# Kernel optimization log

Hardware: AMD Instinct MI355X
Metric: run time of the kernel (lower is better)

## Reference

```python
import jax, jax.numpy as jnp
import numpy as np

T, N, D, E = 4, 50000, 32, 800000
V_TH = 1.0      # v_threshold
ALPHA = 4.0     # surrogate-gradient sharpness


def setup_inputs() -> dict:
    key = jax.random.key(0)
    k1, k2, k3, k4 = jax.random.split(key, 4)
    s_seq = jax.random.normal(k1, (T, N, D), dtype=jnp.float32) * 0.5
    z_seq = jax.random.normal(k2, (N, D), dtype=jnp.float32) * 0.5
    edge_index = jax.random.randint(k3, (2, E), 0, N, dtype=jnp.int64)
    # GCNConv weight (bias=False), Glorot-ish scale
    W = jax.random.normal(k4, (D, D), dtype=jnp.float32) / np.sqrt(D).astype(np.float32)
    return {"s_seq": s_seq, "z_seq": z_seq, "W": W, "edge_index": edge_index}


def _gcn_conv(x, W, edge_index, n_nodes):
    """PyG GCNConv with add_self_loops=True, normalize=True, bias=False.
    x: [T,N,D]; returns [T,N,D]."""
    src, dst = edge_index[0], edge_index[1]
    ones = jnp.ones(src.shape[0], dtype=x.dtype)
    deg = jax.ops.segment_sum(ones, dst, num_segments=n_nodes) + 1.0  # +1 self loop
    dinv = jax.lax.rsqrt(deg)                                        # [N]
    xw = jnp.einsum('tnd,df->tnf', x, W)                             # dense transform
    norm = dinv[src] * dinv[dst]                                     # [E]
    msgs = xw[:, src, :] * norm[None, :, None]                       # [T,E,D] gather
    agg = jax.vmap(lambda m: jax.ops.segment_sum(m, dst, num_segments=n_nodes))(msgs)
    # self-loop contribution with norm dinv[i]^2
    return agg + xw * (dinv * dinv)[None, :, None]


def _spike(v):
    # Heaviside spike with surrogate (sigmoid) gradient, straight-through.
    s = (v >= V_TH).astype(v.dtype)
    sg = jax.nn.sigmoid(ALPHA * (v - V_TH))
    return s + sg - jax.lax.stop_gradient(sg)


def reference(s_seq, z_seq, W, edge_index):
    n_nodes = s_seq.shape[1]
    x_seq = _gcn_conv(s_seq, W, edge_index, n_nodes)   # [T,N,D]  (dropout p=0.0 is identity)
    y_seq = x_seq.mean(0)                              # temporal mean [N,D]
    # Riemannian IF node: integrate-and-fire over time with soft reset;
    # latent state z drifts by the temporal mean (Euclidean proxy for expmap).
    def step(v, x_t):
        v = v + x_t
        o = _spike(v)
        v = v - o * V_TH
        return v, o
    v0 = jnp.zeros_like(z_seq)
    _, o_seq = jax.lax.scan(step, v0, x_seq)           # [T,N,D]
    z_new = z_seq + y_seq
    return o_seq, z_new
```

## Files before the change

### kernel.cpp

```cpp
#include <hip/hip_runtime.h>
#include <hip/hip_fp16.h>

#define TSTEPS 4
#define DIM 32
#define BINW_SHIFT 8
#define NB 256
#define SP_CH 2048
#define NCHP 400
#define PAD_PER_BIN 772

typedef _Float16 f16x8 __attribute__((ext_vector_type(8)));
typedef float f32x4 __attribute__((ext_vector_type(4)));

__device__ __forceinline__ void ldx8h(const __half* p, float4& lo, float4& hi) {
    uint4 u = *(const uint4*)p;
    __half2 h0 = *(__half2*)&u.x;
    __half2 h1 = *(__half2*)&u.y;
    __half2 h2 = *(__half2*)&u.z;
    __half2 h3 = *(__half2*)&u.w;
    float2 a = __half22float2(h0);
    float2 b = __half22float2(h1);
    float2 c = __half22float2(h2);
    float2 d = __half22float2(h3);
    lo = make_float4(a.x, a.y, b.x, b.y);
    hi = make_float4(c.x, c.y, d.x, d.y);
}

__global__ __launch_bounds__(256) void hist_kernel(
    const int* __restrict__ ei, int* __restrict__ ghistT, int E) {
    __shared__ int lh[NB];
    int tid = threadIdx.x;
    lh[tid] = 0;
    __syncthreads();
    int beg = blockIdx.x * SP_CH;
    int end = min(beg + SP_CH, E);
    for (int e = beg + tid; e < end; e += 256)
        atomicAdd(&lh[ei[E + e] >> BINW_SHIFT], 1);
    __syncthreads();
    ghistT[tid * NCHP + blockIdx.x] = lh[tid];
}

__global__ __launch_bounds__(512) void colscan_kernel(
    const int* __restrict__ ghistT, int* __restrict__ ghist2,
    int* __restrict__ totals, int nchunks) {
    __shared__ int sc[512];
    int t = threadIdx.x;
    int b = blockIdx.x;
    int v = (t < nchunks) ? ghistT[b * NCHP + t] : 0;
    sc[t] = v;
    __syncthreads();
    for (int off = 1; off < 512; off <<= 1) {
        int tv = (t >= off) ? sc[t - off] : 0;
        __syncthreads();
        sc[t] += tv;
        __syncthreads();
    }
    if (t < nchunks) ghist2[(size_t)t * NB + b] = sc[t] - v;
    if (t == 511) totals[b] = sc[511];
}

__global__ __launch_bounds__(256) void splitgemm_kernel(
    const int* __restrict__ ei, const int* __restrict__ ghist2,
    const int* __restrict__ totals, unsigned int* __restrict__ esorted,
    int* __restrict__ binScanG,
    const float* __restrict__ s, const float* __restrict__ W,
    __half* __restrict__ xwp, int E, int rows, int N, int nchunks) {
    __shared__ __align__(16) char smem[4352];
    int tid = threadIdx.x;

    if ((int)blockIdx.x < nchunks) {
        int* sBS  = (int*)smem;
        int* gb   = (int*)(smem + 1024);
        int* lcur = (int*)(smem + 2048);
        int bid = blockIdx.x;
        int tot = totals[tid];
        sBS[tid] = tot;
        __syncthreads();
        for (int off = 1; off < 256; off <<= 1) {
            int t = (tid >= off) ? sBS[tid - off] : 0;
            __syncthreads();
            sBS[tid] += t;
            __syncthreads();
        }
        if (bid == 0) binScanG[tid] = sBS[tid];
        gb[tid] = (sBS[tid] - tot) + ghist2[(size_t)bid * NB + tid];
        lcur[tid] = 0;
        __syncthreads();
        int beg = bid * SP_CH;
        int end = min(beg + SP_CH, E);
        for (int e = beg + tid; e < end; e += 256) {
            int sx = ei[e];
            int dx = ei[E + e];
            unsigned int pk = (unsigned int)sx | ((unsigned int)dx << 16);
            int b = dx >> BINW_SHIFT;
            int p = atomicAdd(&lcur[b], 1);
            esorted[gb[b] + p] = pk;
        }
        return;
    }

    float (*Wf)[33] = (float(*)[33])smem;
    {
        float4 wv = ((const float4*)W)[tid];
        int kk = tid >> 3, c4 = (tid & 7) * 4;
        Wf[kk][c4 + 0] = wv.x; Wf[kk][c4 + 1] = wv.y;
        Wf[kk][c4 + 2] = wv.z; Wf[kk][c4 + 3] = wv.w;
    }
    __syncthreads();

    int lane = tid & 63;
    int wid  = tid >> 6;
    int lrow = lane & 15;
    int kq   = lane >> 4;
    int k0   = kq * 8;

    f16x8 b0, b1;
#pragma unroll
    for (int i = 0; i < 8; i++) {
        b0[i] = (_Float16)Wf[k0 + i][lrow];
        b1[i] = (_Float16)Wf[k0 + i][lrow + 16];
    }

    int rbase = ((int)blockIdx.x - nchunks) * 128 + wid * 32;
#pragma unroll
    for (int rt = 0; rt < 2; rt++) {
        int r = rbase + rt * 16 + lrow;
        f16x8 a;
        if (r < rows) {
            const float4* sp = (const float4*)(s + (size_t)r * 32 + k0);
            float4 u0 = sp[0], u1 = sp[1];
            a[0] = (_Float16)u0.x; a[1] = (_Float16)u0.y;
            a[2] = (_Float16)u0.z; a[3] = (_Float16)u0.w;
            a[4] = (_Float16)u1.x; a[5] = (_Float16)u1.y;
            a[6] = (_Float16)u1.z; a[7] = (_Float16)u1.w;
        } else {
#pragma unroll
            for (int i = 0; i < 8; i++) a[i] = (_Float16)0.f;
        }
        f32x4 c0 = {0.f, 0.f, 0.f, 0.f};
        f32x4 c1 = {0.f, 0.f, 0.f, 0.f};
        c0 = __builtin_amdgcn_mfma_f32_16x16x32_f16(b0, a, c0, 0, 0, 0);
        c1 = __builtin_amdgcn_mfma_f32_16x16x32_f16(b1, a, c1, 0, 0, 0);
        if (r < rows) {
            int t = (r >= 3 * N) ? 3 : (r >= 2 * N) ? 2 : (r >= N) ? 1 : 0;
            int n = r - t * N;
            __half2 p0 = __floats2half2_rn(c0[0], c0[1]);
            __half2 p1 = __floats2half2_rn(c0[2], c0[3]);
            __half2 p2 = __floats2half2_rn(c1[0], c1[1]);
            __half2 p3 = __floats2half2_rn(c1[2], c1[3]);
            __half* dst = xwp + (size_t)n * 128 + t * 32;
            uint2 u0, u1;
            u0.x = *(unsigned int*)&p0; u0.y = *(unsigned int*)&p1;
            u1.x = *(unsigned int*)&p2; u1.y = *(unsigned int*)&p3;
            *(uint2*)(dst + kq * 4)      = u0;
            *(uint2*)(dst + 16 + kq * 4) = u1;
        }
    }
}

__global__ __launch_bounds__(512) void csr_kernel(
    const int* __restrict__ binScanG, const unsigned int* __restrict__ esorted,
    int* __restrict__ rec, int* __restrict__ offs, int* __restrict__ deg,
    float* __restrict__ dinv, __half* __restrict__ xwp, int N) {
    __shared__ int lh[NB], sc[NB], loff[NB], lcur[NB];
    __shared__ float sdi[NB];
    int bin = blockIdx.x;
    int tid = threadIdx.x;
    int e0 = bin ? binScanG[bin - 1] : 0;
    int e1 = binScanG[bin];
    int ebeg = e0;
    int cnt = e1 - e0;
    if (tid < NB) lh[tid] = 0;
    __syncthreads();
    int gbase = ((ebeg + 3) & ~3) + PAD_PER_BIN * bin;
    for (int i = tid; i < cnt; i += 512)
        atomicAdd(&lh[(esorted[ebeg + i] >> 16) & 255], 1);
    __syncthreads();
    int padded = 0;
    if (tid < NB) {
        sdi[tid] = rsqrtf((float)lh[tid] + 1.0f);
        padded = (lh[tid] + 3) & ~3;
        sc[tid] = padded;
    }
    __syncthreads();
    for (int off = 1; off < 256; off <<= 1) {
        int t = (tid >= off && tid < NB) ? sc[tid - off] : 0;
        __syncthreads();
        if (tid < NB) sc[tid] += t;
        __syncthreads();
    }
    if (tid < NB) {
        loff[tid] = sc[tid] - padded;
        lcur[tid] = 0;
    }
    __syncthreads();
    for (int i = tid; i < cnt; i += 512) {
        unsigned int e = esorted[ebeg + i];
        int ln = (e >> 16) & 255;
        int p = atomicAdd(&lcur[ln], 1);
        rec[gbase + loff[ln] + p] = (int)(e & 0xFFFFu);
    }
    int n = (bin << BINW_SHIFT) + tid;
    if (tid < NB && n < N) {
        offs[n] = gbase + loff[tid];
        deg[n] = lh[tid];
        dinv[n] = sdi[tid];
    }
    {
        int hbase = bin << 15;
        int limit = min(32768, N * 128 - hbase);
        __half* slab = xwp + hbase;
        for (int i = tid; i * 8 < limit; i += 512) {
            float di = sdi[i >> 4];
            uint4 u = *(uint4*)(slab + i * 8);
            __half2 h0 = *(__half2*)&u.x;
            __half2 h1 = *(__half2*)&u.y;
            __half2 h2 = *(__half2*)&u.z;
            __half2 h3 = *(__half2*)&u.w;
            float2 f0 = __half22float2(h0);
            float2 f1 = __half22float2(h1);
            float2 f2 = __half22float2(h2);
            float2 f3 = __half22float2(h3);
            h0 = __floats2half2_rn(f0.x * di, f0.y * di);
            h1 = __floats2half2_rn(f1.x * di, f1.y * di);
            h2 = __floats2half2_rn(f2.x * di, f2.y * di);
            h3 = __floats2half2_rn(f3.x * di, f3.y * di);
            u.x = *(unsigned int*)&h0;
            u.y = *(unsigned int*)&h1;
            u.z = *(unsigned int*)&h2;
            u.w = *(unsigned int*)&h3;
            *(uint4*)(slab + i * 8) = u;
        }
    }
}

__global__ __launch_bounds__(256) void gather_kernel(
    const int* __restrict__ rec, const int* __restrict__ offs,
    const int* __restrict__ deg, const __half* __restrict__ xwp,
    const float* __restrict__ dinv, const float* __restrict__ z,
    float* __restrict__ out, int N) {
    int gid = blockIdx.x * 256 + threadIdx.x;
    int n = gid >> 4;
    if (n >= N) return;
    int wl = threadIdx.x & 63;
    int g = wl >> 4;
    int l = wl & 15;
    long lofs = (long)l * 8;

    float dn = dinv[n];
    int beg = offs[n];
    int cntn = deg[n];

    float4 aLo = make_float4(0.f, 0.f, 0.f, 0.f);
    float4 aHi = make_float4(0.f, 0.f, 0.f, 0.f);
    int i = 0;
    for (; i + 8 <= cntn; i += 8) {
        int4 sa = *(const int4*)(rec + beg + i);
        int4 sb = *(const int4*)(rec + beg + i + 4);
        float4 l0, h0, l1, h1, l2, h2, l3, h3;
        float4 l4, h4, l5, h5, l6, h6, l7, h7;
        ldx8h(xwp + (long)sa.x * 128 + lofs, l0, h0);
        ldx8h(xwp + (long)sa.y * 128 + lofs, l1, h1);
        ldx8h(xwp + (long)sa.z * 128 + lofs, l2, h2);
        ldx8h(xwp + (long)sa.w * 128 + lofs, l3, h3);
        ldx8h(xwp + (long)sb.x * 128 + lofs, l4, h4);
        ldx8h(xwp + (long)sb.y * 128 + lofs, l5, h5);
        ldx8h(xwp + (long)sb.z * 128 + lofs, l6, h6);
        ldx8h(xwp + (long)sb.w * 128 + lofs, l7, h7);
        aLo.x += (l0.x + l1.x) + (l2.x + l3.x) + (l4.x + l5.x) + (l6.x + l7.x);
        aLo.y += (l0.y + l1.y) + (l2.y + l3.y) + (l4.y + l5.y) + (l6.y + l7.y);
        aLo.z += (l0.z + l1.z) + (l2.z + l3.z) + (l4.z + l5.z) + (l6.z + l7.z);
        aLo.w += (l0.w + l1.w) + (l2.w + l3.w) + (l4.w + l5.w) + (l6.w + l7.w);
        aHi.x += (h0.x + h1.x) + (h2.x + h3.x) + (h4.x + h5.x) + (h6.x + h7.x);
        aHi.y += (h0.y + h1.y) + (h2.y + h3.y) + (h4.y + h5.y) + (h6.y + h7.y);
        aHi.z += (h0.z + h1.z) + (h2.z + h3.z) + (h4.z + h5.z) + (h6.z + h7.z);
        aHi.w += (h0.w + h1.w) + (h2.w + h3.w) + (h4.w + h5.w) + (h6.w + h7.w);
    }
    for (; i < cntn; i += 4) {
        int4 s4 = *(const int4*)(rec + beg + i);
        int rem = cntn - i;
        int i0 = s4.x;
        int i1 = (rem > 1) ? s4.y : i0;
        int i2 = (rem > 2) ? s4.z : i0;
        int i3 = (rem > 3) ? s4.w : i0;
        float w1 = (rem > 1) ? 1.f : 0.f;
        float w2 = (rem > 2) ? 1.f : 0.f;
        float w3 = (rem > 3) ? 1.f : 0.f;
        float4 l0, h0, l1, h1, l2, h2, l3, h3;
        ldx8h(xwp + (long)i0 * 128 + lofs, l0, h0);
        ldx8h(xwp + (long)i1 * 128 + lofs, l1, h1);
        ldx8h(xwp + (long)i2 * 128 + lofs, l2, h2);
        ldx8h(xwp + (long)i3 * 128 + lofs, l3, h3);
        aLo.x += l0.x + w1 * l1.x + w2 * l2.x + w3 * l3.x;
        aLo.y += l0.y + w1 * l1.y + w2 * l2.y + w3 * l3.y;
        aLo.z += l0.z + w1 * l1.z + w2 * l2.z + w3 * l3.z;
        aLo.w += l0.w + w1 * l1.w + w2 * l2.w + w3 * l3.w;
        aHi.x += h0.x + w1 * h1.x + w2 * h2.x + w3 * h3.x;
        aHi.y += h0.y + w1 * h1.y + w2 * h2.y + w3 * h3.y;
        aHi.z += h0.z + w1 * h1.z + w2 * h2.z + w3 * h3.z;
        aHi.w += h0.w + w1 * h1.w + w2 * h2.w + w3 * h3.w;
    }
    {
        float4 sl, sh;
        ldx8h(xwp + (long)n * 128 + lofs, sl, sh);
        aLo.x += sl.x; aLo.y += sl.y; aLo.z += sl.z; aLo.w += sl.w;
        aHi.x += sh.x; aHi.y += sh.y; aHi.z += sh.z; aHi.w += sh.w;
    }
    aLo.x *= dn; aLo.y *= dn; aLo.z *= dn; aLo.w *= dn;
    aHi.x *= dn; aHi.y *= dn; aHi.z *= dn; aHi.w *= dn;

    float a8[8] = {aLo.x, aLo.y, aLo.z, aLo.w, aHi.x, aHi.y, aHi.z, aHi.w};
    float xs[TSTEPS][8];
    int base = g * 16;
#pragma unroll
    for (int t = 0; t < TSTEPS; t++) {
        int srcLane = base + t * 4 + l;
#pragma unroll
        for (int j = 0; j < 8; j++)
            xs[t][j] = __shfl(a8[j], srcLane, 64);
    }
    if (l < 4) {
        int colBase = n * 32 + l * 8;
        float v[8], y[8];
#pragma unroll
        for (int j = 0; j < 8; j++) {
            v[j] = 0.f;
            y[j] = (xs[0][j] + xs[1][j] + xs[2][j] + xs[3][j]) * 0.25f;
        }
#pragma unroll
        for (int t = 0; t < TSTEPS; t++) {
            float o[8];
#pragma unroll
            for (int j = 0; j < 8; j++) {
                v[j] += xs[t][j];
                o[j] = (v[j] >= 1.0f) ? 1.0f : 0.0f;
                v[j] -= o[j];
            }
            float* dst = out + (size_t)t * N * 32 + colBase;
            *(float4*)dst       = make_float4(o[0], o[1], o[2], o[3]);
            *(float4*)(dst + 4) = make_float4(o[4], o[5], o[6], o[7]);
        }
        float4 zv0 = *(const float4*)(z + colBase);
        float4 zv1 = *(const float4*)(z + colBase + 4);
        float* dst = out + (size_t)TSTEPS * N * 32 + colBase;
        *(float4*)dst       = make_float4(zv0.x + y[0], zv0.y + y[1], zv0.z + y[2], zv0.w + y[3]);
        *(float4*)(dst + 4) = make_float4(zv1.x + y[4], zv1.y + y[5], zv1.z + y[6], zv1.w + y[7]);
    }
}

extern "C" void kernel_launch(void* const* d_in, const int* in_sizes, int n_in,
                              void* d_out, int out_size, void* d_ws, size_t ws_size,
                              hipStream_t stream) {
    const float* s_seq = (const float*)d_in[0];
    const float* z_seq = (const float*)d_in[1];
    const float* W     = (const float*)d_in[2];
    const int*   ei    = (const int*)d_in[3];
    float* out = (float*)d_out;

    int N = in_sizes[1] / DIM;
    int E = in_sizes[3] / 2;
    int rows = TSTEPS * N;
    int nb = (N + 255) >> BINW_SHIFT;
    int nchunks = (E + SP_CH - 1) / SP_CH;

    char* w = (char*)d_ws;
    __half* xwp           = (__half*)w;       w += (size_t)rows * DIM * 2;
    unsigned int* esorted = (unsigned int*)w; w += (size_t)E * 4;
    int*   rec     = (int*)w;  w += ((size_t)E + PAD_PER_BIN * nb + 16) * 4;
    int*   offs    = (int*)w;  w += (size_t)N * 4;
    int*   deg     = (int*)w;  w += (size_t)N * 4;
    float* dinv    = (float*)w; w += (size_t)N * 4;
    int*   ghistT  = (int*)w;  w += (size_t)NB * NCHP * 4;
    int*   ghist2  = (int*)w;  w += (size_t)nchunks * NB * 4;
    int*   totals  = (int*)w;  w += NB * 4;
    int*   binScanG = (int*)w; w += NB * 4;

    int xwBlocks = (rows + 127) / 128;
    hist_kernel<<<nchunks, 256, 0, stream>>>(ei, ghistT, E);
    colscan_kernel<<<NB, 512, 0, stream>>>(ghistT, ghist2, totals, nchunks);
    splitgemm_kernel<<<nchunks + xwBlocks, 256, 0, stream>>>(
        ei, ghist2, totals, esorted, binScanG, s_seq, W, xwp, E, rows, N, nchunks);
    csr_kernel<<<nb, 512, 0, stream>>>(binScanG, esorted, rec, offs, deg, dinv,
                                       xwp, N);
    gather_kernel<<<(N * 16 + 255) / 256, 256, 0, stream>>>(rec, offs, deg, xwp,
                                                            dinv, z_seq, out, N);
}
```

Before: 151.1 us.

## Fuse hist/scan/sort/GEMM/CSR kernels into one cooperative persistent kernel

Replaces the four preprocessing kernels (histogram, column scan, split+GEMM, CSR build) with a single cooperative kernel of 256 persistent blocks that separates phases with grid-wide syncs. The edge chunk size doubles, which halves the number of chunks and shrinks the histogram table. Each bin block recomputes the bin prefix scan from totals instead of reading a global binScanG. The aim is to remove launch gaps between dependent kernels. In exchange, fewer blocks are resident, so the GEMM and CSR phases get less parallelism, and the grid syncs add their own cost.

```diff
diff --git a/kernel.cpp b/kernel.cpp
--- a/kernel.cpp
+++ b/kernel.cpp
@@ -1,13 +1,16 @@
 #include <hip/hip_runtime.h>
 #include <hip/hip_fp16.h>
+#include <hip/hip_cooperative_groups.h>
+namespace cg = cooperative_groups;
 
 #define TSTEPS 4
 #define DIM 32
 #define BINW_SHIFT 8
 #define NB 256
-#define SP_CH 2048
-#define NCHP 400
+#define SP_CH 4096
+#define NCHP 256
 #define PAD_PER_BIN 772
+#define GRID 256
 
 typedef _Float16 f16x8 __attribute__((ext_vector_type(8)));
 typedef float f32x4 __attribute__((ext_vector_type(4)));
@@ -26,53 +29,116 @@
     hi = make_float4(c.x, c.y, d.x, d.y);
 }
 
-__global__ __launch_bounds__(256) void hist_kernel(
-    const int* __restrict__ ei, int* __restrict__ ghistT, int E) {
-    __shared__ int lh[NB];
+__global__ __launch_bounds__(256) void pipeline_kernel(
+    const int* __restrict__ ei, int* __restrict__ ghistT,
+    int* __restrict__ ghist2, int* __restrict__ totals,
+    unsigned int* __restrict__ esorted,
+    const float* __restrict__ s, const float* __restrict__ W,
+    __half* __restrict__ xwp,
+    int* __restrict__ rec, int* __restrict__ offs, int* __restrict__ deg,
+    float* __restrict__ dinv,
+    int E, int rows, int N, int nchunks, int ngemm) {
+    cg::grid_group gridg = cg::this_grid();
+    __shared__ float Wf[32][33];
+    __shared__ int scr[4 * NB];
+    __shared__ float sdi[NB];
     int tid = threadIdx.x;
-    lh[tid] = 0;
+    int nbins = (N + 255) >> BINW_SHIFT;
+
+    {
+        float4 wv = ((const float4*)W)[tid];
+        int kk = tid >> 3, c4 = (tid & 7) * 4;
+        Wf[kk][c4 + 0] = wv.x; Wf[kk][c4 + 1] = wv.y;
+        Wf[kk][c4 + 2] = wv.z; Wf[kk][c4 + 3] = wv.w;
+    }
     __syncthreads();
-    int beg = blockIdx.x * SP_CH;
-    int end = min(beg + SP_CH, E);
-    for (int e = beg + tid; e < end; e += 256)
-        atomicAdd(&lh[ei[E + e] >> BINW_SHIFT], 1);
-    __syncthreads();
-    ghistT[tid * NCHP + blockIdx.x] = lh[tid];
-}
-
-__global__ __launch_bounds__(512) void colscan_kernel(
-    const int* __restrict__ ghistT, int* __restrict__ ghist2,
-    int* __restrict__ totals, int nchunks) {
-    __shared__ int sc[512];
-    int t = threadIdx.x;
-    int b = blockIdx.x;
-    int v = (t < nchunks) ? ghistT[b * NCHP + t] : 0;
-    sc[t] = v;
-    __syncthreads();
-    for (int off = 1; off < 512; off <<= 1) {
-        int tv = (t >= off) ? sc[t - off] : 0;
-        __syncthreads();
-        sc[t] += tv;
-        __syncthreads();
-    }
-    if (t < nchunks) ghist2[(size_t)t * NB + b] = sc[t] - v;
-    if (t == 511) totals[b] = sc[511];
-}
-
-__global__ __launch_bounds__(256) void splitgemm_kernel(
-    const int* __restrict__ ei, const int* __restrict__ ghist2,
-    const int* __restrict__ totals, unsigned int* __restrict__ esorted,
-    int* __restrict__ binScanG,
-    const float* __restrict__ s, const float* __restrict__ W,
-    __half* __restrict__ xwp, int E, int rows, int N, int nchunks) {
-    __shared__ __align__(16) char smem[4352];
-    int tid = threadIdx.x;
-
-    if ((int)blockIdx.x < nchunks) {
-        int* sBS  = (int*)smem;
-        int* gb   = (int*)(smem + 1024);
-        int* lcur = (int*)(smem + 2048);
-        int bid = blockIdx.x;
+    int lane = tid & 63;
+    int wid  = tid >> 6;
+    int lrow = lane & 15;
+    int kq   = lane >> 4;
+    int k0   = kq * 8;
+    f16x8 b0, b1;
+#pragma unroll
+    for (int i = 0; i < 8; i++) {
+        b0[i] = (_Float16)Wf[k0 + i][lrow];
+        b1[i] = (_Float16)Wf[k0 + i][lrow + 16];
+    }
+
+    int nwork = nchunks + ngemm;
+    for (int item = blockIdx.x; item < nwork; item += GRID) {
+        if (item < nchunks) {
+            int* lh = scr;
+            lh[tid] = 0;
+            __syncthreads();
+            int beg = item * SP_CH;
+            int end = min(beg + SP_CH, E);
+            for (int e = beg + tid; e < end; e += 256)
+                atomicAdd(&lh[ei[E + e] >> BINW_SHIFT], 1);
+            __syncthreads();
+            ghistT[tid * NCHP + item] = lh[tid];
+            __syncthreads();
+        } else {
+            int tile = item - nchunks;
+            int rbase = tile * 128 + wid * 32;
+#pragma unroll
+            for (int rt = 0; rt < 2; rt++) {
+                int r = rbase + rt * 16 + lrow;
+                f16x8 a;
+                if (r < rows) {
+                    const float4* sp = (const float4*)(s + (size_t)r * 32 + k0);
+                    float4 u0 = sp[0], u1 = sp[1];
+                    a[0] = (_Float16)u0.x; a[1] = (_Float16)u0.y;
+                    a[2] = (_Float16)u0.z; a[3] = (_Float16)u0.w;
+                    a[4] = (_Float16)u1.x; a[5] = (_Float16)u1.y;
+                    a[6] = (_Float16)u1.z; a[7] = (_Float16)u1.w;
+                } else {
+#pragma unroll
+                    for (int i = 0; i < 8; i++) a[i] = (_Float16)0.f;
+                }
+                f32x4 c0 = {0.f, 0.f, 0.f, 0.f};
+                f32x4 c1 = {0.f, 0.f, 0.f, 0.f};
+                c0 = __builtin_amdgcn_mfma_f32_16x16x32_f16(b0, a, c0, 0, 0, 0);
+                c1 = __builtin_amdgcn_mfma_f32_16x16x32_f16(b1, a, c1, 0, 0, 0);
+                if (r < rows) {
+                    int t = (r >= 3 * N) ? 3 : (r >= 2 * N) ? 2 : (r >= N) ? 1 : 0;
+                    int n = r - t * N;
+                    __half2 p0 = __floats2half2_rn(c0[0], c0[1]);
+                    __half2 p1 = __floats2half2_rn(c0[2], c0[3]);
+                    __half2 p2 = __floats2half2_rn(c1[0], c1[1]);
+                    __half2 p3 = __floats2half2_rn(c1[2], c1[3]);
+                    __half* dst = xwp + (size_t)n * 128 + t * 32;
+                    uint2 u0, u1;
+                    u0.x = *(unsigned int*)&p0; u0.y = *(unsigned int*)&p1;
+                    u1.x = *(unsigned int*)&p2; u1.y = *(unsigned int*)&p3;
+                    *(uint2*)(dst + kq * 4)      = u0;
+                    *(uint2*)(dst + 16 + kq * 4) = u1;
+                }
+            }
+        }
+    }
+    gridg.sync();
+
+    if ((int)blockIdx.x < NB) {
+        int b = blockIdx.x;
+        int* sc = scr;
+        int v = (tid < nchunks) ? ghistT[b * NCHP + tid] : 0;
+        sc[tid] = v;
+        __syncthreads();
+        for (int off = 1; off < 256; off <<= 1) {
+            int t = (tid >= off) ? sc[tid - off] : 0;
+            __syncthreads();
+            sc[tid] += t;
+            __syncthreads();
+        }
+        if (tid < nchunks) ghist2[(size_t)tid * NB + b] = sc[tid] - v;
+        if (tid == 255) totals[b] = sc[255];
+    }
+    gridg.sync();
+
+    for (int c = blockIdx.x; c < nchunks; c += GRID) {
+        int* sBS  = scr;
+        int* gb   = scr + NB;
+        int* lcur = scr + 2 * NB;
         int tot = totals[tid];
         sBS[tid] = tot;
         __syncthreads();
@@ -82,11 +148,10 @@
             sBS[tid] += t;
             __syncthreads();
         }
-        if (bid == 0) binScanG[tid] = sBS[tid];
-        gb[tid] = (sBS[tid] - tot) + ghist2[(size_t)bid * NB + tid];
+        gb[tid] = (sBS[tid] - tot) + ghist2[(size_t)c * NB + tid];
         lcur[tid] = 0;
         __syncthreads();
-        int beg = bid * SP_CH;
+        int beg = c * SP_CH;
         int end = min(beg + SP_CH, E);
         for (int e = beg + tid; e < end; e += 256) {
             int sx = ei[e];
@@ -96,141 +161,82 @@
             int p = atomicAdd(&lcur[b], 1);
             esorted[gb[b] + p] = pk;
         }
-        return;
-    }
-
-    float (*Wf)[33] = (float(*)[33])smem;
-    {
-        float4 wv = ((const float4*)W)[tid];
-        int kk = tid >> 3, c4 = (tid & 7) * 4;
-        Wf[kk][c4 + 0] = wv.x; Wf[kk][c4 + 1] = wv.y;
-        Wf[kk][c4 + 2] = wv.z; Wf[kk][c4 + 3] = wv.w;
-    }
-    __syncthreads();
-
-    int lane = tid & 63;
-    int wid  = tid >> 6;
-    int lrow = lane & 15;
-    int kq   = lane >> 4;
-    int k0   = kq * 8;
-
-    f16x8 b0, b1;
-#pragma unroll
-    for (int i = 0; i < 8; i++) {
-        b0[i] = (_Float16)Wf[k0 + i][lrow];
-        b1[i] = (_Float16)Wf[k0 + i][lrow + 16];
-    }
-
-    int rbase = ((int)blockIdx.x - nchunks) * 128 + wid * 32;
-#pragma unroll
-    for (int rt = 0; rt < 2; rt++) {
-        int r = rbase + rt * 16 + lrow;
-        f16x8 a;
-        if (r < rows) {
-            const float4* sp = (const float4*)(s + (size_t)r * 32 + k0);
-            float4 u0 = sp[0], u1 = sp[1];
-            a[0] = (_Float16)u0.x; a[1] = (_Float16)u0.y;
-            a[2] = (_Float16)u0.z; a[3] = (_Float16)u0.w;
-            a[4] = (_Float16)u1.x; a[5] = (_Float16)u1.y;
-            a[6] = (_Float16)u1.z; a[7] = (_Float16)u1.w;
-        } else {
-#pragma unroll
-            for (int i = 0; i < 8; i++) a[i] = (_Float16)0.f;
-        }
-        f32x4 c0 = {0.f, 0.f, 0.f, 0.f};
-        f32x4 c1 = {0.f, 0.f, 0.f, 0.f};
-        c0 = __builtin_amdgcn_mfma_f32_16x16x32_f16(b0, a, c0, 0, 0, 0);
-        c1 = __builtin_amdgcn_mfma_f32_16x16x32_f16(b1, a, c1, 0, 0, 0);
-        if (r < rows) {
-            int t = (r >= 3 * N) ? 3 : (r >= 2 * N) ? 2 : (r >= N) ? 1 : 0;
-            int n = r - t * N;
-            __half2 p0 = __floats2half2_rn(c0[0], c0[1]);
-            __half2 p1 = __floats2half2_rn(c0[2], c0[3]);
-            __half2 p2 = __floats2half2_rn(c1[0], c1[1]);
-            __half2 p3 = __floats2half2_rn(c1[2], c1[3]);
-            __half* dst = xwp + (size_t)n * 128 + t * 32;
-            uint2 u0, u1;
-            u0.x = *(unsigned int*)&p0; u0.y = *(unsigned int*)&p1;
-            u1.x = *(unsigned int*)&p2; u1.y = *(unsigned int*)&p3;
-            *(uint2*)(dst + kq * 4)      = u0;
-            *(uint2*)(dst + 16 + kq * 4) = u1;
-        }
-    }
-}
-
-__global__ __launch_bounds__(512) void csr_kernel(
-    const int* __restrict__ binScanG, const unsigned int* __restrict__ esorted,
-    int* __restrict__ rec, int* __restrict__ offs, int* __restrict__ deg,
-    float* __restrict__ dinv, __half* __restrict__ xwp, int N) {
-    __shared__ int lh[NB], sc[NB], loff[NB], lcur[NB];
-    __shared__ float sdi[NB];
-    int bin = blockIdx.x;
-    int tid = threadIdx.x;
-    int e0 = bin ? binScanG[bin - 1] : 0;
-    int e1 = binScanG[bin];
-    int ebeg = e0;
-    int cnt = e1 - e0;
-    if (tid < NB) lh[tid] = 0;
-    __syncthreads();
-    int gbase = ((ebeg + 3) & ~3) + PAD_PER_BIN * bin;
-    for (int i = tid; i < cnt; i += 512)
-        atomicAdd(&lh[(esorted[ebeg + i] >> 16) & 255], 1);
-    __syncthreads();
-    int padded = 0;
-    if (tid < NB) {
+        __syncthreads();
+    }
+    gridg.sync();
+
+    for (int bin = blockIdx.x; bin < nbins; bin += GRID) {
+        int* lh   = scr;
+        int* sc   = scr + NB;
+        int* loff = scr + 2 * NB;
+        int* lcur = scr + 3 * NB;
+        sc[tid] = totals[tid];
+        lh[tid] = 0;
+        __syncthreads();
+        for (int off = 1; off < 256; off <<= 1) {
+            int t = (tid >= off) ? sc[tid - off] : 0;
+            __syncthreads();
+            sc[tid] += t;
+            __syncthreads();
+        }
+        int e0 = bin ? sc[bin - 1] : 0;
+        int cnt = sc[bin] - e0;
+        int gbase = ((e0 + 3) & ~3) + PAD_PER_BIN * bin;
+        for (int i = tid; i < cnt; i += 256)
+            atomicAdd(&lh[(esorted[e0 + i] >> 16) & 255], 1);
+        __syncthreads();
         sdi[tid] = rsqrtf((float)lh[tid] + 1.0f);
-        padded = (lh[tid] + 3) & ~3;
+        int padded = (lh[tid] + 3) & ~3;
         sc[tid] = padded;
-    }
-    __syncthreads();
-    for (int off = 1; off < 256; off <<= 1) {
-        int t = (tid >= off && tid < NB) ? sc[tid - off] : 0;
-        __syncthreads();
-        if (tid < NB) sc[tid] += t;
-        __syncthreads();
-    }
-    if (tid < NB) {
+        __syncthreads();
+        for (int off = 1; off < 256; off <<= 1) {
+            int t = (tid >= off) ? sc[tid - off] : 0;
+            __syncthreads();
+            sc[tid] += t;
+            __syncthreads();
+        }
         loff[tid] = sc[tid] - padded;
         lcur[tid] = 0;
-    }
-    __syncthreads();
-    for (int i = tid; i < cnt; i += 512) {
-        unsigned int e = esorted[ebeg + i];
-        int ln = (e >> 16) & 255;
-        int p = atomicAdd(&lcur[ln], 1);
-        rec[gbase + loff[ln] + p] = (int)(e & 0xFFFFu);
-    }
-    int n = (bin << BINW_SHIFT) + tid;
-    if (tid < NB && n < N) {
-        offs[n] = gbase + loff[tid];
-        deg[n] = lh[tid];
-        dinv[n] = sdi[tid];
-    }
-    {
-        int hbase = bin << 15;
-        int limit = min(32768, N * 128 - hbase);
-        __half* slab = xwp + hbase;
-        for (int i = tid; i * 8 < limit; i += 512) {
-            float di = sdi[i >> 4];
-            uint4 u = *(uint4*)(slab + i * 8);
-            __half2 h0 = *(__half2*)&u.x;
-            __half2 h1 = *(__half2*)&u.y;
-            __half2 h2 = *(__half2*)&u.z;
-            __half2 h3 = *(__half2*)&u.w;
-            float2 f0 = __half22float2(h0);
-            float2 f1 = __half22float2(h1);
-            float2 f2 = __half22float2(h2);
-            float2 f3 = __half22float2(h3);
-            h0 = __floats2half2_rn(f0.x * di, f0.y * di);
-            h1 = __floats2half2_rn(f1.x * di, f1.y * di);
-            h2 = __floats2half2_rn(f2.x * di, f2.y * di);
-            h3 = __floats2half2_rn(f3.x * di, f3.y * di);
-            u.x = *(unsigned int*)&h0;
-            u.y = *(unsigned int*)&h1;
-            u.z = *(unsigned int*)&h2;
-            u.w = *(unsigned int*)&h3;
-            *(uint4*)(slab + i * 8) = u;
-        }
+        __syncthreads();
+        for (int i = tid; i < cnt; i += 256) {
+            unsigned int e = esorted[e0 + i];
+            int ln = (e >> 16) & 255;
+            int p = atomicAdd(&lcur[ln], 1);
+            rec[gbase + loff[ln] + p] = (int)(e & 0xFFFFu);
+        }
+        int n = (bin << BINW_SHIFT) + tid;
+        if (n < N) {
+            offs[n] = gbase + loff[tid];
+            deg[n] = lh[tid];
+            dinv[n] = sdi[tid];
+        }
+        {
+            int hbase = bin << 15;
+            int limit = min(32768, N * 128 - hbase);
+            __half* slab = xwp + hbase;
+            for (int i = tid; i * 8 < limit; i += 256) {
+                float di = sdi[i >> 4];
+                uint4 u = *(uint4*)(slab + i * 8);
+                __half2 h0 = *(__half2*)&u.x;
+                __half2 h1 = *(__half2*)&u.y;
+                __half2 h2 = *(__half2*)&u.z;
+                __half2 h3 = *(__half2*)&u.w;
+                float2 f0 = __half22float2(h0);
+                float2 f1 = __half22float2(h1);
+                float2 f2 = __half22float2(h2);
+                float2 f3 = __half22float2(h3);
+                h0 = __floats2half2_rn(f0.x * di, f0.y * di);
+                h1 = __floats2half2_rn(f1.x * di, f1.y * di);
+                h2 = __floats2half2_rn(f2.x * di, f2.y * di);
+                h3 = __floats2half2_rn(f3.x * di, f3.y * di);
+                u.x = *(unsigned int*)&h0;
+                u.y = *(unsigned int*)&h1;
+                u.z = *(unsigned int*)&h2;
+                u.w = *(unsigned int*)&h3;
+                *(uint4*)(slab + i * 8) = u;
+            }
+        }
+        __syncthreads();
     }
 }
 
@@ -362,6 +368,7 @@
     int rows = TSTEPS * N;
     int nb = (N + 255) >> BINW_SHIFT;
     int nchunks = (E + SP_CH - 1) / SP_CH;
+    int ngemm = (rows + 127) / 128;
 
     char* w = (char*)d_ws;
     __half* xwp           = (__half*)w;       w += (size_t)rows * DIM * 2;
@@ -373,15 +380,14 @@
     int*   ghistT  = (int*)w;  w += (size_t)NB * NCHP * 4;
     int*   ghist2  = (int*)w;  w += (size_t)nchunks * NB * 4;
     int*   totals  = (int*)w;  w += NB * 4;
-    int*   binScanG = (int*)w; w += NB * 4;
-
-    int xwBlocks = (rows + 127) / 128;
-    hist_kernel<<<nchunks, 256, 0, stream>>>(ei, ghistT, E);
-    colscan_kernel<<<NB, 512, 0, stream>>>(ghistT, ghist2, totals, nchunks);
-    splitgemm_kernel<<<nchunks + xwBlocks, 256, 0, stream>>>(
-        ei, ghist2, totals, esorted, binScanG, s_seq, W, xwp, E, rows, N, nchunks);
-    csr_kernel<<<nb, 512, 0, stream>>>(binScanG, esorted, rec, offs, deg, dinv,
-                                       xwp, N);
+
+    void* args[] = {(void*)&ei, (void*)&ghistT, (void*)&ghist2, (void*)&totals,
+                    (void*)&esorted, (void*)&s_seq, (void*)&W, (void*)&xwp,
+                    (void*)&rec, (void*)&offs, (void*)&deg, (void*)&dinv,
+                    (void*)&E, (void*)&rows, (void*)&N, (void*)&nchunks,
+                    (void*)&ngemm};
+    hipLaunchCooperativeKernel((void*)pipeline_kernel, dim3(GRID), dim3(256),
+                               args, 0, stream);
     gather_kernel<<<(N * 16 + 255) / 256, 256, 0, stream>>>(rec, offs, deg, xwp,
                                                             dinv, z_seq, out, N);
 }
```

Result: slower. 274.4 us (+81.6%).

## Halve node-bin width to double bin count and CSR build parallelism

Applied to the files above, without the earlier changes.

Destination nodes are now bucketed into 128-node bins, giving 391 bins instead of 196. The histogram, scan and scatter kernels move to 512-thread blocks to cover 512 bins, and the GEMM blocks take 256 rows. The aim is more CSR-build blocks so the GPU's compute units are better occupied, and less per-block serial work and shared-memory atomic contention. In exchange the global histogram and scan arrays double in size, and the bin count must stay within 512.

```diff
diff --git a/kernel.cpp b/kernel.cpp
--- a/kernel.cpp
+++ b/kernel.cpp
@@ -3,11 +3,11 @@
 
 #define TSTEPS 4
 #define DIM 32
-#define BINW_SHIFT 8
-#define NB 256
+#define BINW_SHIFT 7
+#define NBN 512
 #define SP_CH 2048
 #define NCHP 400
-#define PAD_PER_BIN 772
+#define PAD_PER_BIN 388
 
 typedef _Float16 f16x8 __attribute__((ext_vector_type(8)));
 typedef float f32x4 __attribute__((ext_vector_type(4)));
@@ -26,15 +26,15 @@
     hi = make_float4(c.x, c.y, d.x, d.y);
 }
 
-__global__ __launch_bounds__(256) void hist_kernel(
+__global__ __launch_bounds__(512) void hist_kernel(
     const int* __restrict__ ei, int* __restrict__ ghistT, int E) {
-    __shared__ int lh[NB];
+    __shared__ int lh[NBN];
     int tid = threadIdx.x;
     lh[tid] = 0;
     __syncthreads();
     int beg = blockIdx.x * SP_CH;
     int end = min(beg + SP_CH, E);
-    for (int e = beg + tid; e < end; e += 256)
+    for (int e = beg + tid; e < end; e += 512)
         atomicAdd(&lh[ei[E + e] >> BINW_SHIFT], 1);
     __syncthreads();
     ghistT[tid * NCHP + blockIdx.x] = lh[tid];
@@ -55,40 +55,40 @@
         sc[t] += tv;
         __syncthreads();
     }
-    if (t < nchunks) ghist2[(size_t)t * NB + b] = sc[t] - v;
+    if (t < nchunks) ghist2[(size_t)t * NBN + b] = sc[t] - v;
     if (t == 511) totals[b] = sc[511];
 }
 
-__global__ __launch_bounds__(256) void splitgemm_kernel(
+__global__ __launch_bounds__(512) void splitgemm_kernel(
     const int* __restrict__ ei, const int* __restrict__ ghist2,
     const int* __restrict__ totals, unsigned int* __restrict__ esorted,
     int* __restrict__ binScanG,
     const float* __restrict__ s, const float* __restrict__ W,
     __half* __restrict__ xwp, int E, int rows, int N, int nchunks) {
-    __shared__ __align__(16) char smem[4352];
+    __shared__ __align__(16) char smem[6144];
     int tid = threadIdx.x;
 
     if ((int)blockIdx.x < nchunks) {
         int* sBS  = (int*)smem;
-        int* gb   = (int*)(smem + 1024);
-        int* lcur = (int*)(smem + 2048);
+        int* gb   = (int*)(smem + 2048);
+        int* lcur = (int*)(smem + 4096);
         int bid = blockIdx.x;
         int tot = totals[tid];
         sBS[tid] = tot;
         __syncthreads();
-        for (int off = 1; off < 256; off <<= 1) {
+        for (int off = 1; off < 512; off <<= 1) {
             int t = (tid >= off) ? sBS[tid - off] : 0;
             __syncthreads();
             sBS[tid] += t;
             __syncthreads();
         }
         if (bid == 0) binScanG[tid] = sBS[tid];
-        gb[tid] = (sBS[tid] - tot) + ghist2[(size_t)bid * NB + tid];
+        gb[tid] = (sBS[tid] - tot) + ghist2[(size_t)bid * NBN + tid];
         lcur[tid] = 0;
         __syncthreads();
         int beg = bid * SP_CH;
         int end = min(beg + SP_CH, E);
-        for (int e = beg + tid; e < end; e += 256) {
+        for (int e = beg + tid; e < end; e += 512) {
             int sx = ei[e];
             int dx = ei[E + e];
             unsigned int pk = (unsigned int)sx | ((unsigned int)dx << 16);
@@ -100,7 +100,7 @@
     }
 
     float (*Wf)[33] = (float(*)[33])smem;
-    {
+    if (tid < 256) {
         float4 wv = ((const float4*)W)[tid];
         int kk = tid >> 3, c4 = (tid & 7) * 4;
         Wf[kk][c4 + 0] = wv.x; Wf[kk][c4 + 1] = wv.y;
@@ -121,7 +121,7 @@
         b1[i] = (_Float16)Wf[k0 + i][lrow + 16];
     }
 
-    int rbase = ((int)blockIdx.x - nchunks) * 128 + wid * 32;
+    int rbase = ((int)blockIdx.x - nchunks) * 256 + wid * 32;
 #pragma unroll
     for (int rt = 0; rt < 2; rt++) {
         int r = rbase + rt * 16 + lrow;
@@ -162,53 +162,53 @@
     const int* __restrict__ binScanG, const unsigned int* __restrict__ esorted,
     int* __restrict__ rec, int* __restrict__ offs, int* __restrict__ deg,
     float* __restrict__ dinv, __half* __restrict__ xwp, int N) {
-    __shared__ int lh[NB], sc[NB], loff[NB], lcur[NB];
-    __shared__ float sdi[NB];
+    __shared__ int lh[128], sc[128], loff[128], lcur[128];
+    __shared__ float sdi[128];
     int bin = blockIdx.x;
     int tid = threadIdx.x;
     int e0 = bin ? binScanG[bin - 1] : 0;
     int e1 = binScanG[bin];
     int ebeg = e0;
     int cnt = e1 - e0;
-    if (tid < NB) lh[tid] = 0;
+    if (tid < 128) lh[tid] = 0;
     __syncthreads();
     int gbase = ((ebeg + 3) & ~3) + PAD_PER_BIN * bin;
     for (int i = tid; i < cnt; i += 512)
-        atomicAdd(&lh[(esorted[ebeg + i] >> 16) & 255], 1);
+        atomicAdd(&lh[(esorted[ebeg + i] >> 16) & 127], 1);
     __syncthreads();
     int padded = 0;
-    if (tid < NB) {
+    if (tid < 128) {
         sdi[tid] = rsqrtf((float)lh[tid] + 1.0f);
         padded = (lh[tid] + 3) & ~3;
         sc[tid] = padded;
     }
     __syncthreads();
-    for (int off = 1; off < 256; off <<= 1) {
-        int t = (tid >= off && tid < NB) ? sc[tid - off] : 0;
-        __syncthreads();
-        if (tid < NB) sc[tid] += t;
-        __syncthreads();
-    }
-    if (tid < NB) {
+    for (int off = 1; off < 128; off <<= 1) {
+        int t = (tid >= off && tid < 128) ? sc[tid - off] : 0;
+        __syncthreads();
+        if (tid < 128) sc[tid] += t;
+        __syncthreads();
+    }
+    if (tid < 128) {
         loff[tid] = sc[tid] - padded;
         lcur[tid] = 0;
     }
     __syncthreads();
     for (int i = tid; i < cnt; i += 512) {
         unsigned int e = esorted[ebeg + i];
-        int ln = (e >> 16) & 255;
+        int ln = (e >> 16) & 127;
         int p = atomicAdd(&lcur[ln], 1);
         rec[gbase + loff[ln] + p] = (int)(e & 0xFFFFu);
     }
     int n = (bin << BINW_SHIFT) + tid;
-    if (tid < NB && n < N) {
+    if (tid < 128 && n < N) {
         offs[n] = gbase + loff[tid];
         deg[n] = lh[tid];
         dinv[n] = sdi[tid];
     }
     {
-        int hbase = bin << 15;
-        int limit = min(32768, N * 128 - hbase);
+        int hbase = bin << 14;
+        int limit = min(16384, N * 128 - hbase);
         __half* slab = xwp + hbase;
         for (int i = tid; i * 8 < limit; i += 512) {
             float di = sdi[i >> 4];
@@ -360,25 +360,25 @@
     int N = in_sizes[1] / DIM;
     int E = in_sizes[3] / 2;
     int rows = TSTEPS * N;
-    int nb = (N + 255) >> BINW_SHIFT;
+    int nb = (N + 127) >> BINW_SHIFT;
     int nchunks = (E + SP_CH - 1) / SP_CH;
 
     char* w = (char*)d_ws;
     __half* xwp           = (__half*)w;       w += (size_t)rows * DIM * 2;
     unsigned int* esorted = (unsigned int*)w; w += (size_t)E * 4;
-    int*   rec     = (int*)w;  w += ((size_t)E + PAD_PER_BIN * nb + 16) * 4;
+    int*   rec     = (int*)w;  w += ((size_t)E + (size_t)PAD_PER_BIN * nb + 16) * 4;
     int*   offs    = (int*)w;  w += (size_t)N * 4;
     int*   deg     = (int*)w;  w += (size_t)N * 4;
     float* dinv    = (float*)w; w += (size_t)N * 4;
-    int*   ghistT  = (int*)w;  w += (size_t)NB * NCHP * 4;
-    int*   ghist2  = (int*)w;  w += (size_t)nchunks * NB * 4;
-    int*   totals  = (int*)w;  w += NB * 4;
-    int*   binScanG = (int*)w; w += NB * 4;
-
-    int xwBlocks = (rows + 127) / 128;
-    hist_kernel<<<nchunks, 256, 0, stream>>>(ei, ghistT, E);
-    colscan_kernel<<<NB, 512, 0, stream>>>(ghistT, ghist2, totals, nchunks);
-    splitgemm_kernel<<<nchunks + xwBlocks, 256, 0, stream>>>(
+    int*   ghistT  = (int*)w;  w += (size_t)NBN * NCHP * 4;
+    int*   ghist2  = (int*)w;  w += (size_t)nchunks * NBN * 4;
+    int*   totals  = (int*)w;  w += NBN * 4;
+    int*   binScanG = (int*)w; w += NBN * 4;
+
+    int xwBlocks = (rows + 255) / 256;
+    hist_kernel<<<nchunks, 512, 0, stream>>>(ei, ghistT, E);
+    colscan_kernel<<<NBN, 512, 0, stream>>>(ghistT, ghist2, totals, nchunks);
+    splitgemm_kernel<<<nchunks + xwBlocks, 512, 0, stream>>>(
         ei, ghist2, totals, esorted, binScanG, s_seq, W, xwp, E, rows, N, nchunks);
     csr_kernel<<<nb, 512, 0, stream>>>(binScanG, esorted, rec, offs, deg, dinv,
                                        xwp, N);
```

Measured after the change: 153.8 us. Within noise of the previous version (+1.8%).
